# Kernel tuning notes

Hardware: AMD Instinct MI355X
Metric: run time of the kernel (lower is better)

Reference implementation:

```python
import jax, jax.numpy as jnp
import numpy as np

EMBED, HEADS, LEVELS, POINTS = 256, 8, 4, 4
HD = EMBED // HEADS
BS, NQ = 2, 16384
SHAPES = [(128, 128), (64, 64), (32, 32), (16, 16)]  # (H, W) per level
NV = sum(h * w for h, w in SHAPES)
EPS = 1e-5


def layernorm(x, g, b):
    mu = jnp.mean(x, -1, keepdims=True)
    var = jnp.mean((x - mu) ** 2, -1, keepdims=True)
    return (x - mu) / jnp.sqrt(var + EPS) * g + b


def bilinear_sample(vl, loc, H, W):
    # vl: (bs, heads, H*W, hd); loc: (bs, nq, heads, P, 2) normalized [0,1]
    # grid_sample semantics: align_corners=False, zero padding
    x = loc[..., 0] * W - 0.5
    y = loc[..., 1] * H - 0.5
    x0 = jnp.floor(x)
    y0 = jnp.floor(y)
    lx, ly = x - x0, y - y0
    x0 = x0.astype(jnp.int32)
    y0 = y0.astype(jnp.int32)
    gather = jax.vmap(jax.vmap(lambda t, i: t[i]))  # over (bs, heads)
    acc = None
    for dx, dy, w in ((0, 0, (1 - lx) * (1 - ly)), (1, 0, lx * (1 - ly)),
                      (0, 1, (1 - lx) * ly), (1, 1, lx * ly)):
        xi, yi = x0 + dx, y0 + dy
        valid = ((xi >= 0) & (xi < W) & (yi >= 0) & (yi < H)).astype(vl.dtype)
        idx = jnp.clip(yi, 0, H - 1) * W + jnp.clip(xi, 0, W - 1)
        idx = idx.transpose(0, 2, 1, 3)           # (bs, heads, nq, P)
        g = gather(vl, idx)                       # (bs, heads, nq, P, hd)
        wv = (w * valid).transpose(0, 2, 1, 3)[..., None]
        acc = g * wv if acc is None else acc + g * wv
    return acc


def forward(lidar_feat, feat_flatten, ref_2d, spatial_shapes, level_start_index,
            q_pose, W_off, b_off, W_attn, b_attn, W_val, b_val, W_out, b_out,
            ln1_g, ln1_b, ffn_w1, ffn_w2, ln2_g, ln2_b):
    identity = lidar_feat                         # (nq, bs, C)
    q = (lidar_feat + q_pose).transpose(1, 0, 2)  # (bs, nq, C)
    bs, nq, C = q.shape
    v = feat_flatten.transpose(1, 0, 2) @ W_val + b_val
    v = v.reshape(bs, -1, HEADS, HD)
    off = (q @ W_off + b_off).reshape(bs, nq, HEADS, LEVELS, POINTS, 2)
    aw = (q @ W_attn + b_attn).reshape(bs, nq, HEADS, LEVELS * POINTS)
    aw = jax.nn.softmax(aw, -1).reshape(bs, nq, HEADS, LEVELS, POINTS)
    ss = np.asarray(spatial_shapes)               # static level shapes
    lsi = np.asarray(level_start_index)
    norm = jnp.asarray(ss[:, ::-1].copy(), q.dtype)  # (L, 2) [W, H]
    loc = ref_2d[:, :, None, :, None, :] + off / norm[None, None, None, :, None, :]
    out = jnp.zeros((bs, nq, HEADS, HD), q.dtype)
    for l in range(LEVELS):
        H, W = int(ss[l, 0]), int(ss[l, 1])
        s = int(lsi[l])
        vl = v[:, s:s + H * W].transpose(0, 2, 1, 3)   # (bs, heads, HW, hd)
        sampled = bilinear_sample(vl, loc[:, :, :, l], H, W)
        out = out + jnp.einsum('bhqpd,bqhp->bqhd', sampled, aw[:, :, :, l, :])
    out = out.reshape(bs, nq, C) @ W_out + b_out
    out = out.transpose(1, 0, 2) + identity       # residual (dropout=eval noop)
    x = layernorm(out, ln1_g, ln1_b)
    x = layernorm(jnp.maximum(x @ ffn_w1, 0.0) @ ffn_w2 + x, ln2_g, ln2_b)
    return x


def setup_inputs():
    key = jax.random.key(0)
    ks = jax.random.split(key, 16)
    starts = np.cumsum([0] + [h * w for h, w in SHAPES])[:-1]
    d = {
        'lidar_feat': jax.random.normal(ks[0], (NQ, BS, EMBED), jnp.float32),
        'feat_flatten': jax.random.normal(ks[1], (NV, BS, EMBED), jnp.float32),
        'ref_2d': jax.random.uniform(ks[2], (BS, NQ, LEVELS, 2), jnp.float32),
        'spatial_shapes': jnp.array(SHAPES, jnp.int32),
        'level_start_index': jnp.array(starts, jnp.int32),
        'q_pose': jax.random.normal(ks[3], (NQ, BS, EMBED), jnp.float32),
        'W_off': 0.02 * jax.random.normal(ks[4], (EMBED, HEADS * LEVELS * POINTS * 2), jnp.float32),
        'b_off': 2.0 * jax.random.normal(ks[5], (HEADS * LEVELS * POINTS * 2,), jnp.float32),
        'W_attn': 0.02 * jax.random.normal(ks[6], (EMBED, HEADS * LEVELS * POINTS), jnp.float32),
        'b_attn': jnp.zeros((HEADS * LEVELS * POINTS,), jnp.float32),
        'W_val': 0.02 * jax.random.normal(ks[7], (EMBED, EMBED), jnp.float32),
        'b_val': jnp.zeros((EMBED,), jnp.float32),
        'W_out': 0.02 * jax.random.normal(ks[8], (EMBED, EMBED), jnp.float32),
        'b_out': jnp.zeros((EMBED,), jnp.float32),
        'ln1_g': jnp.ones((EMBED,), jnp.float32),
        'ln1_b': jnp.zeros((EMBED,), jnp.float32),
        'ffn_w1': 0.02 * jax.random.normal(ks[9], (EMBED, EMBED), jnp.float32),
        'ffn_w2': 0.02 * jax.random.normal(ks[10], (EMBED, EMBED), jnp.float32),
        'ln2_g': jnp.ones((EMBED,), jnp.float32),
        'ln2_b': jnp.zeros((EMBED,), jnp.float32),
    }
    return d


def reference(lidar_feat, feat_flatten, ref_2d, spatial_shapes, level_start_index,
              q_pose, W_off, b_off, W_attn, b_attn, W_val, b_val, W_out, b_out,
              ln1_g, ln1_b, ffn_w1, ffn_w2, ln2_g, ln2_b):
    return forward(lidar_feat, feat_flatten, ref_2d, spatial_shapes,
                   level_start_index, q_pose, W_off, b_off, W_attn, b_attn,
                   W_val, b_val, W_out, b_out, ln1_g, ln1_b, ffn_w1, ffn_w2,
                   ln2_g, ln2_b)
```

## Files before the change

### kernel.cpp

```cpp
#include <hip/hip_runtime.h>
#include <cstdint>

#define EMBED 256
#define HEADS 8
#define LEVELS 4
#define POINTS 4
#define BS 2
#define NQ 16384
#define NV 21760
#define MQ (BS*NQ)
#define MV (BS*NV)
#define VAL_BLK 340
#define OA_BLK  256

typedef __attribute__((ext_vector_type(8))) short short8;
typedef __attribute__((ext_vector_type(4))) float f32x4;

__device__ __forceinline__ unsigned short f2bf(float f) {
    unsigned int u = __float_as_uint(f);
    u = (u + 0x7FFFu + ((u >> 16) & 1u)) >> 16;
    return (unsigned short)u;
}
__device__ __forceinline__ float bf2f(unsigned short h) {
    return __uint_as_float(((unsigned int)h) << 16);
}
__device__ __forceinline__ void glds16(const unsigned short* g, unsigned short* l) {
    __builtin_amdgcn_global_load_lds((const __attribute__((address_space(1))) void*)g,
                                     (__attribute__((address_space(3))) void*)l, 16, 0, 0);
}

struct WtArgs {
    const float* src[6];
    unsigned short* dst[6];
    int n[6];
};
__global__ __launch_bounds__(256) void prep_wt(
    WtArgs a, const float* __restrict__ ref2d,
    int* __restrict__ bkt, int* __restrict__ hist)
{
    const int t = threadIdx.x, g = blockIdx.y, bx = blockIdx.x;
    if (g == 6) {
        if (bx < 64) {
#pragma unroll
            for (int i = 0; i < 2; ++i) {
                const int rb = bx * 512 + i * 256 + t;
                const float x = ref2d[(size_t)rb * 8 + 0];
                const float y = ref2d[(size_t)rb * 8 + 1];
                const int qx = min(15, max(0, (int)(x * 16.f)));
                const int qy = min(15, max(0, (int)(y * 16.f)));
                const int bv = (rb >> 14) * 256 + qy * 16 + qx;
                bkt[rb] = bv;
                atomicAdd(&hist[bv], 1);
            }
        }
        return;
    }
    const int N = a.n[g];
    const int e = bx * 256 + t;
    if (e >= 256 * N) return;
    const int k = e / N, n = e - k * N;
    a.dst[g][(size_t)n * 256 + k] = f2bf(a.src[g][e]);
}

template<int NCOLS>
__device__ __forceinline__ void gemm_core(
    unsigned short* As, unsigned short* Bs, int bx,
    const float* __restrict__ Af, const float* __restrict__ A2f, int inner,
    const unsigned short* __restrict__ Bt,
    const float* __restrict__ bias0, const float* __restrict__ bias1,
    unsigned short* __restrict__ lidarb, unsigned short* __restrict__ outh)
{
    constexpr int FN = NCOLS / 64;
    const int t = threadIdx.x, l = t & 63, w = t >> 6;
    const int wm = w >> 2, wn = w & 3;
    const int frow = l & 15, fgrp = l >> 4;
    const size_t brow = (size_t)bx * 128;

    const int fslot = fgrp ^ ((frow & 3) ^ ((frow >> 2) & 3));
    const int srow = l >> 2;
    const int sswz = (l & 3) ^ ((srow & 3) ^ ((srow >> 2) & 3));
    const unsigned short* gB0 = Bt + ((size_t)(w * 16 + srow)) * 256 + sswz * 8;

    const int arow_s = t >> 2, aslot_s = t & 3;
    const int grow = (int)brow + arow_s;
    const int bidx = grow / inner, nn = grow - bidx * inner;
    const size_t srcrow = (size_t)(nn * BS + bidx) * 256;
    const float* srcA = Af + srcrow;
    const float* srcA2 = A2f ? A2f + srcrow : nullptr;
    const int aswz_s = aslot_s ^ ((arow_s & 3) ^ ((arow_s >> 2) & 3));

    f32x4 acc[4][FN];
#pragma unroll
    for (int i = 0; i < 4; ++i)
#pragma unroll
        for (int j = 0; j < FN; ++j) acc[i][j] = f32x4{0.f, 0.f, 0.f, 0.f};

    float4 pA0 = *(const float4*)(srcA + aslot_s * 8);
    float4 pA1 = *(const float4*)(srcA + aslot_s * 8 + 4);
    float4 pC0, pC1;
    if (srcA2) { pC0 = *(const float4*)(srcA2 + aslot_s * 8);
                 pC1 = *(const float4*)(srcA2 + aslot_s * 8 + 4); }

    for (int k0 = 0; k0 < 256; k0 += 32) {
        glds16(gB0 + k0,         &Bs[w * 512]);
        glds16(gB0 + 32768 + k0, &Bs[(w + 8) * 512]);
        if constexpr (NCOLS == 384)
            glds16(gB0 + 65536 + k0, &Bs[(w + 16) * 512]);

        if (lidarb) {
            short8 lk;
            lk[0] = (short)f2bf(pA0.x); lk[1] = (short)f2bf(pA0.y);
            lk[2] = (short)f2bf(pA0.z); lk[3] = (short)f2bf(pA0.w);
            lk[4] = (short)f2bf(pA1.x); lk[5] = (short)f2bf(pA1.y);
            lk[6] = (short)f2bf(pA1.z); lk[7] = (short)f2bf(pA1.w);
            *reinterpret_cast<short8*>(lidarb + srcrow + k0 + aslot_s * 8) = lk;
        }

        float c[8] = {pA0.x, pA0.y, pA0.z, pA0.w, pA1.x, pA1.y, pA1.z, pA1.w};
        if (srcA2) {
            c[0] += pC0.x; c[1] += pC0.y; c[2] += pC0.z; c[3] += pC0.w;
            c[4] += pC1.x; c[5] += pC1.y; c[6] += pC1.z; c[7] += pC1.w;
        }
        short8 pk;
#pragma unroll
        for (int i = 0; i < 8; ++i) pk[i] = (short)f2bf(c[i]);
        *reinterpret_cast<short8*>(&As[arow_s * 32 + aswz_s * 8]) = pk;
        if (k0 + 32 < 256) {
            pA0 = *(const float4*)(srcA + k0 + 32 + aslot_s * 8);
            pA1 = *(const float4*)(srcA + k0 + 32 + aslot_s * 8 + 4);
            if (srcA2) { pC0 = *(const float4*)(srcA2 + k0 + 32 + aslot_s * 8);
                         pC1 = *(const float4*)(srcA2 + k0 + 32 + aslot_s * 8 + 4); }
        }
        __syncthreads();

        short8 af[4]; short8 bq[FN];
#pragma unroll
        for (int fm = 0; fm < 4; ++fm)
            af[fm] = *reinterpret_cast<const short8*>(&As[(wm * 64 + fm * 16 + frow) * 32 + fslot * 8]);
#pragma unroll
        for (int fn = 0; fn < FN; ++fn)
            bq[fn] = *reinterpret_cast<const short8*>(&Bs[(wn * (NCOLS / 4) + fn * 16 + frow) * 32 + fslot * 8]);
#pragma unroll
        for (int fm = 0; fm < 4; ++fm)
#pragma unroll
            for (int fn = 0; fn < FN; ++fn)
                acc[fm][fn] = __builtin_amdgcn_mfma_f32_16x16x32_bf16(af[fm], bq[fn], acc[fm][fn], 0, 0, 0);
        __syncthreads();
    }

#pragma unroll
    for (int fn = 0; fn < FN; ++fn) {
        const int col = wn * (NCOLS / 4) + fn * 16 + frow;
        float b = 0.f;
        if (NCOLS == 384) b = (col < 256) ? bias0[col] : bias1[col - 256];
        else              b = bias0[col];
#pragma unroll
        for (int fm = 0; fm < 4; ++fm)
#pragma unroll
            for (int j = 0; j < 4; ++j) {
                const size_t row = brow + wm * 64 + fm * 16 + fgrp * 4 + j;
                outh[row * NCOLS + col] = f2bf(acc[fm][fn][j] + b);
            }
    }
}

__global__ __launch_bounds__(512) void valoa_k(
    const float* __restrict__ feat, const float* __restrict__ lidar,
    const float* __restrict__ q_pose,
    const unsigned short* __restrict__ wt_val, const unsigned short* __restrict__ wt_oa,
    const float* __restrict__ b_val, const float* __restrict__ b_off,
    const float* __restrict__ b_attn,
    unsigned short* __restrict__ vb, unsigned short* __restrict__ oa,
    unsigned short* __restrict__ lidarb,
    const int* __restrict__ hist, const int* __restrict__ bkt,
    int* __restrict__ perm)
{
    __shared__ unsigned short As[128 * 32];
    __shared__ unsigned short Bs[384 * 32];
    const int bx = blockIdx.x;
    if (bx < VAL_BLK) {
        gemm_core<256>(As, Bs, bx, feat, nullptr, NV, wt_val, b_val, nullptr, nullptr, vb);
    } else if (bx < VAL_BLK + OA_BLK) {
        gemm_core<384>(As, Bs, bx - VAL_BLK, lidar, q_pose, NQ, wt_oa, b_off, b_attn, lidarb, oa);
    } else {
        int* s   = (int*)As;
        int* cur = ((int*)As) + 512;
        const int t = threadIdx.x;
        const int v = hist[t];
        s[t] = v;
        __syncthreads();
        int acc = v;
#pragma unroll
        for (int o = 1; o < 512; o <<= 1) {
            const int add = (t >= o) ? s[t - o] : 0;
            __syncthreads();
            acc += add;
            s[t] = acc;
            __syncthreads();
        }
        cur[t] = acc - v;
        __syncthreads();
#pragma unroll 4
        for (int i = 0; i < 64; ++i) {
            const int rb = i * 512 + t;
            const int pos = atomicAdd(&cur[bkt[rb]], 1);
            perm[pos] = rb;
        }
    }
}

__global__ __launch_bounds__(256, 8) void sampler_k(
    const unsigned short* __restrict__ oa,
    const float* __restrict__ ref2d,
    const unsigned short* __restrict__ v,
    const int* __restrict__ perm,
    unsigned short* __restrict__ outh)
{
    const int bid = blockIdx.x;
    const int sbid = (bid & 7) * (MQ / 4 / 8) + (bid >> 3);
    const int q0 = sbid * 4;
    const int t = threadIdx.x;
    const int tq = t >> 6;
    const int l = t & 63;

    __shared__ uint2 s_d[4][8][4][17];

    const int rb = perm[q0 + tq];
    const int b = rb >> 14, qi = rb & (NQ - 1);

#pragma unroll
    for (int it = 0; it < 2; ++it) {
        const int hlp = it * 64 + l;
        const int h = hlp >> 4, lp = hlp & 15, li = lp >> 2;

        const float2 refv = *(const float2*)(ref2d + (size_t)rb * 8 + li * 2);
        const ushort2 offu = *(const ushort2*)(oa + (size_t)rb * 384 + hlp * 2);
        const float ax = bf2f(oa[(size_t)rb * 384 + 256 + hlp]);

        float m = ax;
#pragma unroll
        for (int o = 1; o < 16; o <<= 1) m = fmaxf(m, __shfl_xor(m, o));
        const float e = __expf(ax - m);
        float sden = e;
#pragma unroll
        for (int o = 1; o < 16; o <<= 1) sden += __shfl_xor(sden, o);
        const float a = e / sden;

        const int Wl[4]  = {128, 64, 32, 16};
        const int S0l[4] = {0, 16384, 20480, 21504};
        const int Wi = Wl[li]; const float Wf = (float)Wi;
        const float x = (refv.x + bf2f(offu.x) / Wf) * Wf - 0.5f;
        const float y = (refv.y + bf2f(offu.y) / Wf) * Wf - 0.5f;
        const float x0f = floorf(x), y0f = floorf(y);
        const float lx = x - x0f, ly = y - y0f;
        const int x0 = (int)x0f, y0 = (int)y0f;
        const float cw[4] = {(1.f - lx) * (1.f - ly) * a, lx * (1.f - ly) * a,
                             (1.f - lx) * ly * a,          lx * ly * a};
        const int base = b * NV + S0l[li];
#pragma unroll
        for (int c = 0; c < 4; ++c) {
            const int xi = x0 + (c & 1), yi = y0 + (c >> 1);
            const bool val = (xi >= 0) & (xi < Wi) & (yi >= 0) & (yi < Wi);
            const int xc = min(max(xi, 0), Wi - 1), yc = min(max(yi, 0), Wi - 1);
            const unsigned int ofs = (unsigned int)(base + yc * Wi + xc) * 512u + h * 64u;
            s_d[tq][h][c][lp] = make_uint2(__float_as_uint(val ? cw[c] : 0.f), ofs);
        }
    }

    asm volatile("s_waitcnt lgkmcnt(0)" ::: "memory");
    __builtin_amdgcn_sched_barrier(0);

    const int h = l >> 3, dq = l & 7;
    const char* vq = (const char*)v + dq * 8u;
    const uint2* dp = &s_d[tq][h][0][0];
    float a0 = 0.f, a1 = 0.f, a2 = 0.f, a3 = 0.f;
#pragma unroll
    for (int c = 0; c < 4; ++c) {
#pragma unroll
        for (int i = 0; i < 16; ++i) {
            const uint2 dd = dp[c * 17 + i];
            const uint2 raw = *(const uint2*)(vq + dd.y);
            const float wgt = __uint_as_float(dd.x);
            a0 += wgt * __uint_as_float(raw.x << 16);
            a1 += wgt * __uint_as_float(raw.x & 0xFFFF0000u);
            a2 += wgt * __uint_as_float(raw.y << 16);
            a3 += wgt * __uint_as_float(raw.y & 0xFFFF0000u);
        }
    }
    ushort4 o; o.x = f2bf(a0); o.y = f2bf(a1); o.z = f2bf(a2); o.w = f2bf(a3);
    *(ushort4*)(outh + (size_t)(qi * BS + b) * 256 + h * 32 + dq * 4) = o;
}

__global__ __launch_bounds__(512) void mega_k(
    const unsigned short* __restrict__ smp, const unsigned short* __restrict__ lidarb,
    const unsigned short* __restrict__ Wo, const unsigned short* __restrict__ W1,
    const unsigned short* __restrict__ W2, const float* __restrict__ b_out,
    const float* __restrict__ ln1g, const float* __restrict__ ln1b,
    const float* __restrict__ ln2g, const float* __restrict__ ln2b,
    float* __restrict__ outf)
{
    __shared__ unsigned short XH[64 * 256];
    __shared__ unsigned short Bs[256 * 32];
    __shared__ float2 sdLN[64][4];

    const int t = threadIdx.x, l = t & 63, w = t >> 6;
    const int wm = w >> 2, wn = w & 3;
    const int frow = l & 15, fgrp = l >> 4;
    const size_t brow = (size_t)blockIdx.x * 64;

    const int fslot = fgrp ^ ((frow & 3) ^ ((frow >> 2) & 3));
    const int srow = l >> 2;
    const int sswz = (l & 3) ^ ((srow & 3) ^ ((srow >> 2) & 3));

    const unsigned short* gA  = smp + (brow + (size_t)((w & 3) * 16 + srow)) * 256 + sswz * 8;
    const unsigned short* gWo = Wo + ((size_t)(w * 16 + srow)) * 256 + sswz * 8;
    const unsigned short* gW1 = W1 + ((size_t)(w * 16 + srow)) * 256 + sswz * 8;
    const unsigned short* gW2 = W2 + ((size_t)(w * 16 + srow)) * 256 + sswz * 8;

    f32x4 acc[2][4];
    f32x4 xres[2][4];

#pragma unroll
    for (int i = 0; i < 2; ++i)
#pragma unroll
        for (int j = 0; j < 4; ++j) acc[i][j] = f32x4{0.f, 0.f, 0.f, 0.f};

    for (int k0 = 0; k0 < 256; k0 += 32) {
        glds16(gWo + k0,         &Bs[w * 512]);
        glds16(gWo + 32768 + k0, &Bs[(w + 8) * 512]);
        if (w < 4) glds16(gA + k0, &XH[w * 512]);
        __syncthreads();
        short8 af[2], bq[4];
#pragma unroll
        for (int fm = 0; fm < 2; ++fm)
            af[fm] = *reinterpret_cast<const short8*>(&XH[(wm * 32 + fm * 16 + frow) * 32 + fslot * 8]);
#pragma unroll
        for (int fn = 0; fn < 4; ++fn)
            bq[fn] = *reinterpret_cast<const short8*>(&Bs[(wn * 64 + fn * 16 + frow) * 32 + fslot * 8]);
#pragma unroll
        for (int fm = 0; fm < 2; ++fm)
#pragma unroll
            for (int fn = 0; fn < 4; ++fn)
                acc[fm][fn] = __builtin_amdgcn_mfma_f32_16x16x32_bf16(af[fm], bq[fn], acc[fm][fn], 0, 0, 0);
        __syncthreads();
    }

#pragma unroll
    for (int fm = 0; fm < 2; ++fm)
#pragma unroll
        for (int fn = 0; fn < 4; ++fn) {
            const int col = wn * 64 + fn * 16 + frow;
            const float bv = b_out[col];
#pragma unroll
            for (int j = 0; j < 4; ++j) {
                const size_t row = brow + wm * 32 + fm * 16 + fgrp * 4 + j;
                acc[fm][fn][j] += bv + bf2f(lidarb[row * 256 + col]);
            }
        }
#pragma unroll
    for (int fm = 0; fm < 2; ++fm)
#pragma unroll
        for (int j = 0; j < 4; ++j) {
            float s1 = 0.f, s2 = 0.f;
#pragma unroll
            for (int fn = 0; fn < 4; ++fn) { const float x = acc[fm][fn][j]; s1 += x; s2 += x * x; }
#pragma unroll
            for (int o = 1; o < 16; o <<= 1) { s1 += __shfl_xor(s1, o); s2 += __shfl_xor(s2, o); }
            if (frow == 0) sdLN[wm * 32 + fm * 16 + fgrp * 4 + j][wn] = make_float2(s1, s2);
        }
    __syncthreads();
#pragma unroll
    for (int fm = 0; fm < 2; ++fm)
#pragma unroll
        for (int j = 0; j < 4; ++j) {
            const int rl = wm * 32 + fm * 16 + fgrp * 4 + j;
            const float2 p0 = sdLN[rl][0], p1 = sdLN[rl][1], p2 = sdLN[rl][2], p3 = sdLN[rl][3];
            const float s1 = p0.x + p1.x + p2.x + p3.x;
            const float s2 = p0.y + p1.y + p2.y + p3.y;
            const float mu = s1 * (1.f / 256.f);
            const float var = s2 * (1.f / 256.f) - mu * mu;
            const float rstd = rsqrtf(var + 1e-5f);
#pragma unroll
            for (int fn = 0; fn < 4; ++fn) {
                const int col = wn * 64 + fn * 16 + frow;
                const float y = (acc[fm][fn][j] - mu) * rstd * ln1g[col] + ln1b[col];
                xres[fm][fn][j] = y;
                const int ss = (col >> 3) ^ (rl & 7);
                XH[rl * 256 + ss * 8 + (col & 7)] = f2bf(y);
            }
        }
    __syncthreads();

#pragma unroll
    for (int i = 0; i < 2; ++i)
#pragma unroll
        for (int j = 0; j < 4; ++j) acc[i][j] = f32x4{0.f, 0.f, 0.f, 0.f};

    for (int k0 = 0; k0 < 256; k0 += 32) {
        glds16(gW1 + k0,         &Bs[w * 512]);
        glds16(gW1 + 32768 + k0, &Bs[(w + 8) * 512]);
        __syncthreads();
        short8 af[2], bq[4];
#pragma unroll
        for (int fm = 0; fm < 2; ++fm) {
            const int row = wm * 32 + fm * 16 + frow;
            const int ss = ((k0 >> 3) + fgrp) ^ (row & 7);
            af[fm] = *reinterpret_cast<const short8*>(&XH[row * 256 + ss * 8]);
        }
#pragma unroll
        for (int fn = 0; fn < 4; ++fn)
            bq[fn] = *reinterpret_cast<const short8*>(&Bs[(wn * 64 + fn * 16 + frow) * 32 + fslot * 8]);
#pragma unroll
        for (int fm = 0; fm < 2; ++fm)
#pragma unroll
            for (int fn = 0; fn < 4; ++fn)
                acc[fm][fn] = __builtin_amdgcn_mfma_f32_16x16x32_bf16(af[fm], bq[fn], acc[fm][fn], 0, 0, 0);
        __syncthreads();
    }

#pragma unroll
    for (int fm = 0; fm < 2; ++fm)
#pragma unroll
        for (int fn = 0; fn < 4; ++fn) {
            const int col = wn * 64 + fn * 16 + frow;
#pragma unroll
            for (int j = 0; j < 4; ++j) {
                const int rl = wm * 32 + fm * 16 + fgrp * 4 + j;
                const int ss = (col >> 3) ^ (rl & 7);
                XH[rl * 256 + ss * 8 + (col & 7)] = f2bf(fmaxf(acc[fm][fn][j], 0.f));
            }
        }
    __syncthreads();

#pragma unroll
    for (int i = 0; i < 2; ++i)
#pragma unroll
        for (int j = 0; j < 4; ++j) acc[i][j] = f32x4{0.f, 0.f, 0.f, 0.f};

    for (int k0 = 0; k0 < 256; k0 += 32) {
        glds16(gW2 + k0,         &Bs[w * 512]);
        glds16(gW2 + 32768 + k0, &Bs[(w + 8) * 512]);
        __syncthreads();
        short8 af[2], bq[4];
#pragma unroll
        for (int fm = 0; fm < 2; ++fm) {
            const int row = wm * 32 + fm * 16 + frow;
            const int ss = ((k0 >> 3) + fgrp) ^ (row & 7);
            af[fm] = *reinterpret_cast<const short8*>(&XH[row * 256 + ss * 8]);
        }
#pragma unroll
        for (int fn = 0; fn < 4; ++fn)
            bq[fn] = *reinterpret_cast<const short8*>(&Bs[(wn * 64 + fn * 16 + frow) * 32 + fslot * 8]);
#pragma unroll
        for (int fm = 0; fm < 2; ++fm)
#pragma unroll
            for (int fn = 0; fn < 4; ++fn)
                acc[fm][fn] = __builtin_amdgcn_mfma_f32_16x16x32_bf16(af[fm], bq[fn], acc[fm][fn], 0, 0, 0);
        __syncthreads();
    }

#pragma unroll
    for (int fm = 0; fm < 2; ++fm)
#pragma unroll
        for (int fn = 0; fn < 4; ++fn)
#pragma unroll
            for (int j = 0; j < 4; ++j) acc[fm][fn][j] += xres[fm][fn][j];
#pragma unroll
    for (int fm = 0; fm < 2; ++fm)
#pragma unroll
        for (int j = 0; j < 4; ++j) {
            float s1 = 0.f, s2 = 0.f;
#pragma unroll
            for (int fn = 0; fn < 4; ++fn) { const float x = acc[fm][fn][j]; s1 += x; s2 += x * x; }
#pragma unroll
            for (int o = 1; o < 16; o <<= 1) { s1 += __shfl_xor(s1, o); s2 += __shfl_xor(s2, o); }
            if (frow == 0) sdLN[wm * 32 + fm * 16 + fgrp * 4 + j][wn] = make_float2(s1, s2);
        }
    __syncthreads();
#pragma unroll
    for (int fm = 0; fm < 2; ++fm)
#pragma unroll
        for (int j = 0; j < 4; ++j) {
            const int rl = wm * 32 + fm * 16 + fgrp * 4 + j;
            const float2 p0 = sdLN[rl][0], p1 = sdLN[rl][1], p2 = sdLN[rl][2], p3 = sdLN[rl][3];
            const float s1 = p0.x + p1.x + p2.x + p3.x;
            const float s2 = p0.y + p1.y + p2.y + p3.y;
            const float mu = s1 * (1.f / 256.f);
            const float var = s2 * (1.f / 256.f) - mu * mu;
            const float rstd = rsqrtf(var + 1e-5f);
            const size_t row = brow + rl;
#pragma unroll
            for (int fn = 0; fn < 4; ++fn) {
                const int col = wn * 64 + fn * 16 + frow;
                outf[row * 256 + col] = (acc[fm][fn][j] - mu) * rstd * ln2g[col] + ln2b[col];
            }
        }
}

extern "C" void kernel_launch(void* const* d_in, const int* in_sizes, int n_in,
                              void* d_out, int out_size, void* d_ws, size_t ws_size,
                              hipStream_t stream)
{
    const float* lidar  = (const float*)d_in[0];
    const float* feat   = (const float*)d_in[1];
    const float* ref2d  = (const float*)d_in[2];
    const float* q_pose = (const float*)d_in[5];
    const float* W_off  = (const float*)d_in[6];
    const float* b_off  = (const float*)d_in[7];
    const float* W_attn = (const float*)d_in[8];
    const float* b_attn = (const float*)d_in[9];
    const float* W_val  = (const float*)d_in[10];
    const float* b_val  = (const float*)d_in[11];
    const float* W_out  = (const float*)d_in[12];
    const float* b_out  = (const float*)d_in[13];
    const float* ln1_g  = (const float*)d_in[14];
    const float* ln1_b  = (const float*)d_in[15];
    const float* ffn_w1 = (const float*)d_in[16];
    const float* ffn_w2 = (const float*)d_in[17];
    const float* ln2_g  = (const float*)d_in[18];
    const float* ln2_b  = (const float*)d_in[19];

    float* out = (float*)d_out;
    char*  ws  = (char*)d_ws;

    unsigned short* vb     = (unsigned short*)(ws + 0);
    unsigned short* oa     = (unsigned short*)(ws + 22282240);
    unsigned short* smp    = (unsigned short*)(ws + 47448064);
    unsigned short* lidarb = (unsigned short*)(ws + 64225280);
    unsigned short* wt     = (unsigned short*)(ws + 81002496);
    int* perm = (int*)(ws + 81723392);
    int* bkt  = (int*)(ws + 81854464);
    int* hist = (int*)(ws + 81985536);
    unsigned short* wt_val = wt;
    unsigned short* wt_oa  = wt + 65536;
    unsigned short* wt_out = wt + 163840;
    unsigned short* wt_f1  = wt + 229376;
    unsigned short* wt_f2  = wt + 294912;

    WtArgs wa;
    wa.src[0] = W_val;  wa.dst[0] = wt_val;          wa.n[0] = 256;
    wa.src[1] = W_off;  wa.dst[1] = wt_oa;           wa.n[1] = 256;
    wa.src[2] = W_attn; wa.dst[2] = wt_oa + 65536;   wa.n[2] = 128;
    wa.src[3] = W_out;  wa.dst[3] = wt_out;          wa.n[3] = 256;
    wa.src[4] = ffn_w1; wa.dst[4] = wt_f1;           wa.n[4] = 256;
    wa.src[5] = ffn_w2; wa.dst[5] = wt_f2;           wa.n[5] = 256;

    hipMemsetAsync(hist, 0, 2048, stream);

    prep_wt<<<dim3(384, 7), dim3(256), 0, stream>>>(wa, ref2d, bkt, hist);

    valoa_k<<<dim3(VAL_BLK + OA_BLK + 1), dim3(512), 0, stream>>>(
        feat, lidar, q_pose, wt_val, wt_oa, b_val, b_off, b_attn,
        vb, oa, lidarb, hist, bkt, perm);

    sampler_k<<<dim3(MQ / 4), dim3(256), 0, stream>>>(oa, ref2d, vb, perm, smp);

    mega_k<<<dim3(MQ / 64), dim3(512), 0, stream>>>(
        smp, lidarb, wt_out, wt_f1, wt_f2, b_out,
        ln1_g, ln1_b, ln2_g, ln2_b, out);
}
```

Before: 229.8 us.

## Split fused output-projection/FFN megakernel into separate outproj and FFN kernels

```diff
diff --git a/kernel.cpp b/kernel.cpp
--- a/kernel.cpp
+++ b/kernel.cpp
@@ -209,7 +209,7 @@
     }
 }
 
-__global__ __launch_bounds__(256, 8) void sampler_k(
+__global__ __launch_bounds__(256) void sampler_k(
     const unsigned short* __restrict__ oa,
     const float* __restrict__ ref2d,
     const unsigned short* __restrict__ v,
@@ -220,18 +220,16 @@
     const int sbid = (bid & 7) * (MQ / 4 / 8) + (bid >> 3);
     const int q0 = sbid * 4;
     const int t = threadIdx.x;
-    const int tq = t >> 6;
-    const int l = t & 63;
 
     __shared__ uint2 s_d[4][8][4][17];
 
-    const int rb = perm[q0 + tq];
-    const int b = rb >> 14, qi = rb & (NQ - 1);
-
 #pragma unroll
     for (int it = 0; it < 2; ++it) {
-        const int hlp = it * 64 + l;
+        const int item = t + it * 256;
+        const int tq = item >> 7, hlp = item & 127;
         const int h = hlp >> 4, lp = hlp & 15, li = lp >> 2;
+        const int rb = perm[q0 + tq];
+        const int b = rb >> 14;
 
         const float2 refv = *(const float2*)(ref2d + (size_t)rb * 8 + li * 2);
         const ushort2 offu = *(const ushort2*)(oa + (size_t)rb * 384 + hlp * 2);
@@ -262,24 +260,22 @@
             const int xi = x0 + (c & 1), yi = y0 + (c >> 1);
             const bool val = (xi >= 0) & (xi < Wi) & (yi >= 0) & (yi < Wi);
             const int xc = min(max(xi, 0), Wi - 1), yc = min(max(yi, 0), Wi - 1);
-            const unsigned int ofs = (unsigned int)(base + yc * Wi + xc) * 512u + h * 64u;
+            const unsigned int ofs = (unsigned int)(base + yc * Wi + xc) * 256u + h * 32;
             s_d[tq][h][c][lp] = make_uint2(__float_as_uint(val ? cw[c] : 0.f), ofs);
         }
     }
-
-    asm volatile("s_waitcnt lgkmcnt(0)" ::: "memory");
-    __builtin_amdgcn_sched_barrier(0);
-
-    const int h = l >> 3, dq = l & 7;
-    const char* vq = (const char*)v + dq * 8u;
-    const uint2* dp = &s_d[tq][h][0][0];
+    __syncthreads();
+
+    const int tq = t >> 6, l = t & 63, h = l >> 3, dq = l & 7;
+    const int rb = perm[q0 + tq], b = rb >> 14, qi = rb & (NQ - 1);
+    const unsigned short* vd = v + dq * 4;
     float a0 = 0.f, a1 = 0.f, a2 = 0.f, a3 = 0.f;
 #pragma unroll
     for (int c = 0; c < 4; ++c) {
 #pragma unroll
         for (int i = 0; i < 16; ++i) {
-            const uint2 dd = dp[c * 17 + i];
-            const uint2 raw = *(const uint2*)(vq + dd.y);
+            const uint2 dd = s_d[tq][h][c][i];
+            const uint2 raw = *(const uint2*)(vd + dd.y);
             const float wgt = __uint_as_float(dd.x);
             a0 += wgt * __uint_as_float(raw.x << 16);
             a1 += wgt * __uint_as_float(raw.x & 0xFFFF0000u);
@@ -291,74 +287,71 @@
     *(ushort4*)(outh + (size_t)(qi * BS + b) * 256 + h * 32 + dq * 4) = o;
 }
 
-__global__ __launch_bounds__(512) void mega_k(
+__global__ __launch_bounds__(512) void outproj_k(
     const unsigned short* __restrict__ smp, const unsigned short* __restrict__ lidarb,
-    const unsigned short* __restrict__ Wo, const unsigned short* __restrict__ W1,
-    const unsigned short* __restrict__ W2, const float* __restrict__ b_out,
+    const unsigned short* __restrict__ Wo, const float* __restrict__ b_out,
     const float* __restrict__ ln1g, const float* __restrict__ ln1b,
-    const float* __restrict__ ln2g, const float* __restrict__ ln2b,
-    float* __restrict__ outf)
-{
-    __shared__ unsigned short XH[64 * 256];
+    unsigned short* __restrict__ xln)
+{
+    __shared__ unsigned short As[128 * 32];
     __shared__ unsigned short Bs[256 * 32];
-    __shared__ float2 sdLN[64][4];
+    __shared__ float2 sdLN[128][4];
 
     const int t = threadIdx.x, l = t & 63, w = t >> 6;
     const int wm = w >> 2, wn = w & 3;
     const int frow = l & 15, fgrp = l >> 4;
-    const size_t brow = (size_t)blockIdx.x * 64;
+    const size_t brow = (size_t)blockIdx.x * 128;
 
     const int fslot = fgrp ^ ((frow & 3) ^ ((frow >> 2) & 3));
     const int srow = l >> 2;
     const int sswz = (l & 3) ^ ((srow & 3) ^ ((srow >> 2) & 3));
 
-    const unsigned short* gA  = smp + (brow + (size_t)((w & 3) * 16 + srow)) * 256 + sswz * 8;
-    const unsigned short* gWo = Wo + ((size_t)(w * 16 + srow)) * 256 + sswz * 8;
-    const unsigned short* gW1 = W1 + ((size_t)(w * 16 + srow)) * 256 + sswz * 8;
-    const unsigned short* gW2 = W2 + ((size_t)(w * 16 + srow)) * 256 + sswz * 8;
-
-    f32x4 acc[2][4];
-    f32x4 xres[2][4];
-
-#pragma unroll
-    for (int i = 0; i < 2; ++i)
+    const unsigned short* gA = smp + (brow + (size_t)(w * 16 + srow)) * 256 + sswz * 8;
+    const unsigned short* gB = Wo + ((size_t)(w * 16 + srow)) * 256 + sswz * 8;
+
+    f32x4 acc[4][4];
+#pragma unroll
+    for (int i = 0; i < 4; ++i)
 #pragma unroll
         for (int j = 0; j < 4; ++j) acc[i][j] = f32x4{0.f, 0.f, 0.f, 0.f};
 
     for (int k0 = 0; k0 < 256; k0 += 32) {
-        glds16(gWo + k0,         &Bs[w * 512]);
-        glds16(gWo + 32768 + k0, &Bs[(w + 8) * 512]);
-        if (w < 4) glds16(gA + k0, &XH[w * 512]);
-        __syncthreads();
-        short8 af[2], bq[4];
-#pragma unroll
-        for (int fm = 0; fm < 2; ++fm)
-            af[fm] = *reinterpret_cast<const short8*>(&XH[(wm * 32 + fm * 16 + frow) * 32 + fslot * 8]);
+        glds16(gB + k0,         &Bs[w * 512]);
+        glds16(gB + 32768 + k0, &Bs[(w + 8) * 512]);
+        glds16(gA + k0, &As[w * 512]);
+        __syncthreads();
+
+        short8 af[4], bq[4];
+#pragma unroll
+        for (int fm = 0; fm < 4; ++fm)
+            af[fm] = *reinterpret_cast<const short8*>(&As[(wm * 64 + fm * 16 + frow) * 32 + fslot * 8]);
 #pragma unroll
         for (int fn = 0; fn < 4; ++fn)
             bq[fn] = *reinterpret_cast<const short8*>(&Bs[(wn * 64 + fn * 16 + frow) * 32 + fslot * 8]);
 #pragma unroll
-        for (int fm = 0; fm < 2; ++fm)
+        for (int fm = 0; fm < 4; ++fm)
 #pragma unroll
             for (int fn = 0; fn < 4; ++fn)
                 acc[fm][fn] = __builtin_amdgcn_mfma_f32_16x16x32_bf16(af[fm], bq[fn], acc[fm][fn], 0, 0, 0);
         __syncthreads();
     }
 
-#pragma unroll
-    for (int fm = 0; fm < 2; ++fm)
-#pragma unroll
-        for (int fn = 0; fn < 4; ++fn) {
-            const int col = wn * 64 + fn * 16 + frow;
-            const float bv = b_out[col];
-#pragma unroll
-            for (int j = 0; j < 4; ++j) {
-                const size_t row = brow + wm * 32 + fm * 16 + fgrp * 4 + j;
-                acc[fm][fn][j] += bv + bf2f(lidarb[row * 256 + col]);
-            }
-        }
-#pragma unroll
-    for (int fm = 0; fm < 2; ++fm)
+    int cols[4];
+#pragma unroll
+    for (int fn = 0; fn < 4; ++fn) cols[fn] = wn * 64 + fn * 16 + frow;
+
+#pragma unroll
+    for (int fm = 0; fm < 4; ++fm)
+#pragma unroll
+        for (int j = 0; j < 4; ++j) {
+            const size_t row = brow + wm * 64 + fm * 16 + fgrp * 4 + j;
+#pragma unroll
+            for (int fn = 0; fn < 4; ++fn)
+                acc[fm][fn][j] += b_out[cols[fn]] + bf2f(lidarb[row * 256 + cols[fn]]);
+        }
+
+#pragma unroll
+    for (int fm = 0; fm < 4; ++fm)
 #pragma unroll
         for (int j = 0; j < 4; ++j) {
             float s1 = 0.f, s2 = 0.f;
@@ -366,30 +359,56 @@
             for (int fn = 0; fn < 4; ++fn) { const float x = acc[fm][fn][j]; s1 += x; s2 += x * x; }
 #pragma unroll
             for (int o = 1; o < 16; o <<= 1) { s1 += __shfl_xor(s1, o); s2 += __shfl_xor(s2, o); }
-            if (frow == 0) sdLN[wm * 32 + fm * 16 + fgrp * 4 + j][wn] = make_float2(s1, s2);
+            if (frow == 0)
+                sdLN[wm * 64 + fm * 16 + fgrp * 4 + j][wn] = make_float2(s1, s2);
         }
     __syncthreads();
-#pragma unroll
-    for (int fm = 0; fm < 2; ++fm)
+    float gv[4], bv[4];
+#pragma unroll
+    for (int fn = 0; fn < 4; ++fn) { gv[fn] = ln1g[cols[fn]]; bv[fn] = ln1b[cols[fn]]; }
+#pragma unroll
+    for (int fm = 0; fm < 4; ++fm)
 #pragma unroll
         for (int j = 0; j < 4; ++j) {
-            const int rl = wm * 32 + fm * 16 + fgrp * 4 + j;
+            const int rl = wm * 64 + fm * 16 + fgrp * 4 + j;
             const float2 p0 = sdLN[rl][0], p1 = sdLN[rl][1], p2 = sdLN[rl][2], p3 = sdLN[rl][3];
             const float s1 = p0.x + p1.x + p2.x + p3.x;
             const float s2 = p0.y + p1.y + p2.y + p3.y;
             const float mu = s1 * (1.f / 256.f);
             const float var = s2 * (1.f / 256.f) - mu * mu;
             const float rstd = rsqrtf(var + 1e-5f);
-#pragma unroll
-            for (int fn = 0; fn < 4; ++fn) {
-                const int col = wn * 64 + fn * 16 + frow;
-                const float y = (acc[fm][fn][j] - mu) * rstd * ln1g[col] + ln1b[col];
-                xres[fm][fn][j] = y;
-                const int ss = (col >> 3) ^ (rl & 7);
-                XH[rl * 256 + ss * 8 + (col & 7)] = f2bf(y);
-            }
-        }
-    __syncthreads();
+            const size_t row = brow + rl;
+#pragma unroll
+            for (int fn = 0; fn < 4; ++fn)
+                xln[row * 256 + cols[fn]] = f2bf((acc[fm][fn][j] - mu) * rstd * gv[fn] + bv[fn]);
+        }
+}
+
+__global__ __launch_bounds__(512) void ffn_fused(
+    const unsigned short* __restrict__ X,
+    const unsigned short* __restrict__ W1t, const unsigned short* __restrict__ W2t,
+    const float* __restrict__ lng, const float* __restrict__ lnb,
+    float* __restrict__ outf)
+{
+    __shared__ unsigned short As[64 * 32];
+    __shared__ unsigned short Bs[256 * 32];
+    __shared__ unsigned short Hs[64 * 256];
+    __shared__ float2 sdLN[64][4];
+
+    const int t = threadIdx.x, l = t & 63, w = t >> 6;
+    const int wm = w >> 2, wn = w & 3;
+    const int frow = l & 15, fgrp = l >> 4;
+    const size_t brow = (size_t)blockIdx.x * 64;
+
+    const int fslot = fgrp ^ ((frow & 3) ^ ((frow >> 2) & 3));
+    const int srow = l >> 2;
+    const int sswz = (l & 3) ^ ((srow & 3) ^ ((srow >> 2) & 3));
+
+    const unsigned short* gX  = X + (brow + (size_t)((w & 3) * 16 + srow)) * 256 + sswz * 8;
+    const unsigned short* gW1 = W1t + ((size_t)(w * 16 + srow)) * 256 + sswz * 8;
+    const unsigned short* gW2 = W2t + ((size_t)(w * 16 + srow)) * 256 + sswz * 8;
+
+    f32x4 acc[2][4];
 
 #pragma unroll
     for (int i = 0; i < 2; ++i)
@@ -399,14 +418,13 @@
     for (int k0 = 0; k0 < 256; k0 += 32) {
         glds16(gW1 + k0,         &Bs[w * 512]);
         glds16(gW1 + 32768 + k0, &Bs[(w + 8) * 512]);
-        __syncthreads();
+        if (w < 4) glds16(gX + k0, &As[w * 512]);
+        __syncthreads();
+
         short8 af[2], bq[4];
 #pragma unroll
-        for (int fm = 0; fm < 2; ++fm) {
-            const int row = wm * 32 + fm * 16 + frow;
-            const int ss = ((k0 >> 3) + fgrp) ^ (row & 7);
-            af[fm] = *reinterpret_cast<const short8*>(&XH[row * 256 + ss * 8]);
-        }
+        for (int fm = 0; fm < 2; ++fm)
+            af[fm] = *reinterpret_cast<const short8*>(&As[(wm * 32 + fm * 16 + frow) * 32 + fslot * 8]);
 #pragma unroll
         for (int fn = 0; fn < 4; ++fn)
             bq[fn] = *reinterpret_cast<const short8*>(&Bs[(wn * 64 + fn * 16 + frow) * 32 + fslot * 8]);
@@ -425,9 +443,9 @@
             const int col = wn * 64 + fn * 16 + frow;
 #pragma unroll
             for (int j = 0; j < 4; ++j) {
-                const int rl = wm * 32 + fm * 16 + fgrp * 4 + j;
-                const int ss = (col >> 3) ^ (rl & 7);
-                XH[rl * 256 + ss * 8 + (col & 7)] = f2bf(fmaxf(acc[fm][fn][j], 0.f));
+                const int row = wm * 32 + fm * 16 + fgrp * 4 + j;
+                const int ss = (col >> 3) ^ (row & 7);
+                Hs[row * 256 + ss * 8 + (col & 7)] = f2bf(fmaxf(acc[fm][fn][j], 0.f));
             }
         }
     __syncthreads();
@@ -441,12 +459,14 @@
         glds16(gW2 + k0,         &Bs[w * 512]);
         glds16(gW2 + 32768 + k0, &Bs[(w + 8) * 512]);
         __syncthreads();
+
         short8 af[2], bq[4];
 #pragma unroll
         for (int fm = 0; fm < 2; ++fm) {
             const int row = wm * 32 + fm * 16 + frow;
-            const int ss = ((k0 >> 3) + fgrp) ^ (row & 7);
-            af[fm] = *reinterpret_cast<const short8*>(&XH[row * 256 + ss * 8]);
+            const int ksg = (k0 >> 3) + fgrp;
+            const int ss = ksg ^ (row & 7);
+            af[fm] = *reinterpret_cast<const short8*>(&Hs[row * 256 + ss * 8]);
         }
 #pragma unroll
         for (int fn = 0; fn < 4; ++fn)
@@ -462,9 +482,14 @@
 #pragma unroll
     for (int fm = 0; fm < 2; ++fm)
 #pragma unroll
-        for (int fn = 0; fn < 4; ++fn)
-#pragma unroll
-            for (int j = 0; j < 4; ++j) acc[fm][fn][j] += xres[fm][fn][j];
+        for (int fn = 0; fn < 4; ++fn) {
+            const int col = wn * 64 + fn * 16 + frow;
+#pragma unroll
+            for (int j = 0; j < 4; ++j) {
+                const size_t row = brow + wm * 32 + fm * 16 + fgrp * 4 + j;
+                acc[fm][fn][j] += bf2f(X[row * 256 + col]);
+            }
+        }
 #pragma unroll
     for (int fm = 0; fm < 2; ++fm)
 #pragma unroll
@@ -474,7 +499,8 @@
             for (int fn = 0; fn < 4; ++fn) { const float x = acc[fm][fn][j]; s1 += x; s2 += x * x; }
 #pragma unroll
             for (int o = 1; o < 16; o <<= 1) { s1 += __shfl_xor(s1, o); s2 += __shfl_xor(s2, o); }
-            if (frow == 0) sdLN[wm * 32 + fm * 16 + fgrp * 4 + j][wn] = make_float2(s1, s2);
+            if (frow == 0)
+                sdLN[wm * 32 + fm * 16 + fgrp * 4 + j][wn] = make_float2(s1, s2);
         }
     __syncthreads();
 #pragma unroll
@@ -492,7 +518,7 @@
 #pragma unroll
             for (int fn = 0; fn < 4; ++fn) {
                 const int col = wn * 64 + fn * 16 + frow;
-                outf[row * 256 + col] = (acc[fm][fn][j] - mu) * rstd * ln2g[col] + ln2b[col];
+                outf[row * 256 + col] = (acc[fm][fn][j] - mu) * rstd * lng[col] + lnb[col];
             }
         }
 }
@@ -526,11 +552,12 @@
     unsigned short* vb     = (unsigned short*)(ws + 0);
     unsigned short* oa     = (unsigned short*)(ws + 22282240);
     unsigned short* smp    = (unsigned short*)(ws + 47448064);
-    unsigned short* lidarb = (unsigned short*)(ws + 64225280);
-    unsigned short* wt     = (unsigned short*)(ws + 81002496);
-    int* perm = (int*)(ws + 81723392);
-    int* bkt  = (int*)(ws + 81854464);
-    int* hist = (int*)(ws + 81985536);
+    unsigned short* xln    = (unsigned short*)(ws + 64225280);
+    unsigned short* lidarb = (unsigned short*)(ws + 81002496);
+    unsigned short* wt     = (unsigned short*)(ws + 97779712);
+    int* perm = (int*)(ws + 98500608);
+    int* bkt  = (int*)(ws + 98631680);
+    int* hist = (int*)(ws + 98762752);
     unsigned short* wt_val = wt;
     unsigned short* wt_oa  = wt + 65536;
     unsigned short* wt_out = wt + 163840;
@@ -555,7 +582,9 @@
 
     sampler_k<<<dim3(MQ / 4), dim3(256), 0, stream>>>(oa, ref2d, vb, perm, smp);
 
-    mega_k<<<dim3(MQ / 64), dim3(512), 0, stream>>>(
-        smp, lidarb, wt_out, wt_f1, wt_f2, b_out,
-        ln1_g, ln1_b, ln2_g, ln2_b, out);
-}
+    outproj_k<<<dim3(MQ / 128), dim3(512), 0, stream>>>(
+        smp, lidarb, wt_out, b_out, ln1_g, ln1_b, xln);
+
+    ffn_fused<<<dim3(MQ / 64), dim3(512), 0, stream>>>(
+        xln, wt_f1, wt_f2, ln2_g, ln2_b, out);
+}
```

Measured after the change: 198.4 us. -13.7%, faster.
